# Performance work log

Measured on AMD Instinct MI355X. Metric: run time of the kernel, lower is better.

## Reference

```python
import jax, jax.numpy as jnp
import numpy as np

B, T, E, H = 16, 1024, 1024, 16
DH = E // H  # 64, divisible by 4
THETA = 10000.0


def setup_inputs() -> dict:
    key = jax.random.key(0)
    ks = jax.random.split(key, 10)
    inp = {
        "hidden_states": jax.random.normal(ks[0], (B, T, E), dtype=jnp.float32),
        "rope_pos": jax.random.randint(ks[1], (B, T, 2), 0, 32, dtype=jnp.int32),
    }
    s = 0.02
    inp["Wq"] = jax.random.normal(ks[2], (E, E), dtype=jnp.float32) * s
    inp["bq"] = jnp.zeros((E,), dtype=jnp.float32)
    inp["Wk"] = jax.random.normal(ks[3], (E, E), dtype=jnp.float32) * s
    inp["bk"] = jnp.zeros((E,), dtype=jnp.float32)
    inp["Wv"] = jax.random.normal(ks[4], (E, E), dtype=jnp.float32) * s
    inp["bv"] = jnp.zeros((E,), dtype=jnp.float32)
    inp["Wo"] = jax.random.normal(ks[5], (E, E), dtype=jnp.float32) * s
    inp["bo"] = jnp.zeros((E,), dtype=jnp.float32)
    return inp


def _rotate_half(x):
    # interleaved pairs: (x0,x1,x2,x3,...) -> (-x1,x0,-x3,x2,...)
    x_even = x[..., ::2]
    x_odd = x[..., 1::2]
    return jnp.stack((-x_odd, x_even), axis=-1).reshape(x.shape)


def _apply_rope_2d(q, k, rope_pos, theta):
    Dh = q.shape[-1]
    half, quarter = Dh // 2, Dh // 4
    dtype = q.dtype
    idx = jnp.arange(quarter, dtype=dtype)
    inv = (theta ** (-2.0 * idx / quarter)).astype(dtype)  # [quarter]
    pos_h = rope_pos[..., 0].astype(dtype)[..., None]  # [B,T,1]
    pos_w = rope_pos[..., 1].astype(dtype)[..., None]
    ang_h = pos_h * inv  # [B,T,quarter]
    ang_w = pos_w * inv
    ri = lambda a: jnp.repeat(a, 2, axis=-1)[:, None]  # -> [B,1,T,half]
    cos_h, sin_h = ri(jnp.cos(ang_h)), ri(jnp.sin(ang_h))
    cos_w, sin_w = ri(jnp.cos(ang_w)), ri(jnp.sin(ang_w))
    q_h, q_w = q[..., :half], q[..., half:]
    k_h, k_w = k[..., :half], k[..., half:]
    q_h = q_h * cos_h + _rotate_half(q_h) * sin_h
    k_h = k_h * cos_h + _rotate_half(k_h) * sin_h
    q_w = q_w * cos_w + _rotate_half(q_w) * sin_w
    k_w = k_w * cos_w + _rotate_half(k_w) * sin_w
    return jnp.concatenate([q_h, q_w], axis=-1), jnp.concatenate([k_h, k_w], axis=-1)


def reference(hidden_states, rope_pos, Wq, bq, Wk, bk, Wv, bv, Wo, bo):
    b, t, e = hidden_states.shape
    scale = DH ** -0.5
    # torch nn.Linear: y = x @ W.T + b, W is [out, in]
    proj = lambda x, W, bias: jnp.einsum('bte,oe->bto', x, W) + bias
    q = proj(hidden_states, Wq, bq).reshape(b, t, H, DH).transpose(0, 2, 1, 3)
    k = proj(hidden_states, Wk, bk).reshape(b, t, H, DH).transpose(0, 2, 1, 3)
    v = proj(hidden_states, Wv, bv).reshape(b, t, H, DH).transpose(0, 2, 1, 3)
    q, k = _apply_rope_2d(q, k, rope_pos, THETA)
    # eager attention: scores in input dtype, softmax in float32
    scores = jnp.einsum('bhqd,bhkd->bhqk', q, k) * scale
    w = jax.nn.softmax(scores.astype(jnp.float32), axis=-1).astype(q.dtype)
    out = jnp.einsum('bhqk,bhkd->bhqd', w, v)
    out = out.transpose(0, 2, 1, 3).reshape(b, t, e)
    return jnp.einsum('bte,oe->bto', out, Wo) + bo
```

## Files before the change

### kernel.cpp

```cpp
#include <hip/hip_runtime.h>
#include <hip/hip_bf16.h>

#define B_  16
#define T_  1024
#define E_  1024
#define H_  16
#define DH_ 64

typedef short s16x8 __attribute__((ext_vector_type(8)));
typedef float f32x4 __attribute__((ext_vector_type(4)));
typedef unsigned short u16x4 __attribute__((ext_vector_type(4)));

__device__ __forceinline__ void async_cp16(const void* g, void* l) {
  __builtin_amdgcn_global_load_lds(
      (__attribute__((address_space(1))) unsigned int*)(g),
      (__attribute__((address_space(3))) unsigned int*)(l), 16, 0, 0);
}

__device__ __forceinline__ s16x8 frag8(const void* p) { return *(const s16x8*)p; }

__device__ __forceinline__ float fexp2(float x) {
#if __has_builtin(__builtin_amdgcn_exp2f)
  return __builtin_amdgcn_exp2f(x);
#else
  return exp2f(x);
#endif
}

__device__ __forceinline__ unsigned short f2bu(float x) {
  __hip_bfloat16 h = __float2bfloat16(x);
  return *reinterpret_cast<unsigned short*>(&h);
}

__global__ __launch_bounds__(256) void cast_all(const float* __restrict__ X,
                                                const float* __restrict__ Wq,
                                                const float* __restrict__ Wk,
                                                const float* __restrict__ Wv,
                                                const float* __restrict__ Wo,
                                                __hip_bfloat16* __restrict__ Xb,
                                                __hip_bfloat16* __restrict__ Wqkvb,
                                                __hip_bfloat16* __restrict__ Wob) {
  const int bid = blockIdx.x;
  const float* src;
  __hip_bfloat16* dst;
  int i;
  if (bid < 16384) {
    src = X; dst = Xb;
    i = ((bid & 7) * 2048 + (bid >> 3)) * 256 + threadIdx.x;
  } else {
    const int wb = bid - 16384;
    const int w = wb >> 10;
    src = (w == 0) ? Wq : (w == 1) ? Wk : (w == 2) ? Wv : Wo;
    dst = (w == 3) ? Wob : Wqkvb + (size_t)w * 1048576;
    i = (wb & 1023) * 256 + threadIdx.x;
  }
  float4 v = ((const float4*)src)[i];
  u16x4 pk = {f2bu(v.x), f2bu(v.y), f2bu(v.z), f2bu(v.w)};
  *(u16x4*)(dst + (size_t)i * 4) = pk;
}

#define G8_ISSUE(SRC_, LOFF_, H_, D_, KT_)                                      \
  {                                                                             \
    _Pragma("unroll") for (int u_ = 0; u_ < 2; ++u_) {                          \
      const int ch_ = u_ * 8 + wave;                                            \
      async_cp16(SRC_ + (size_t)((H_)*128 + ch_ * 8) * 2048 + (KT_)*128,        \
                 smem + (D_)*65536 + (LOFF_) + (H_)*16384 + ch_ * 1024);        \
    }                                                                           \
  }

#define G8_READ_A(D_, S_)                                                       \
  {                                                                             \
    _Pragma("unroll") for (int i_ = 0; i_ < 4; ++i_) {                          \
      const char* rp_ = smem + (D_)*65536 + wrow * 16384 +                      \
                        ((S_)*64 + i_ * 16 + col) * 128;                        \
      af[i_][0] = frag8(rp_ + sw0);                                             \
      af[i_][1] = frag8(rp_ + sw1);                                             \
    }                                                                           \
  }

#define G8_READ_B(D_, T8_, BF_)                                                 \
  {                                                                             \
    _Pragma("unroll") for (int j_ = 0; j_ < 2; ++j_) {                          \
      const char* rp_ = smem + (D_)*65536 + 32768 + (wcol >> 1) * 16384 +       \
                        ((wcol & 1) * 64 + (T8_)*32 + j_ * 16 + col) * 128;     \
      BF_[j_][0] = frag8(rp_ + sw0);                                            \
      BF_[j_][1] = frag8(rp_ + sw1);                                            \
    }                                                                           \
  }

#define G8_MFMA(S_, T8_, BF_)                                                   \
  {                                                                             \
    __builtin_amdgcn_s_setprio(1);                                              \
    _Pragma("unroll") for (int i_ = 0; i_ < 4; ++i_)                            \
      _Pragma("unroll") for (int j_ = 0; j_ < 2; ++j_) {                        \
        acc[(S_)*4 + i_][(T8_)*2 + j_] = __builtin_amdgcn_mfma_f32_16x16x32_bf16( \
            af[i_][0], BF_[j_][0], acc[(S_)*4 + i_][(T8_)*2 + j_], 0, 0, 0);    \
        acc[(S_)*4 + i_][(T8_)*2 + j_] = __builtin_amdgcn_mfma_f32_16x16x32_bf16( \
            af[i_][1], BF_[j_][1], acc[(S_)*4 + i_][(T8_)*2 + j_], 0, 0, 0);    \
      }                                                                         \
    __builtin_amdgcn_s_setprio(0);                                              \
  }

#define G8_KTILE(D_, GA_, GB_, KTA_, KTB_, VM_)                                 \
  G8_READ_A(D_, 0)                                                              \
  G8_READ_B(D_, 0, bf0)                                                         \
  if (GA_) G8_ISSUE(Asrc, 0, 0, (D_) ^ 1, KTA_)                                 \
  __builtin_amdgcn_s_barrier();                                                 \
  G8_MFMA(0, 0, bf0)                                                            \
  __builtin_amdgcn_s_barrier();                                                 \
  G8_READ_B(D_, 1, bf1)                                                         \
  if (GA_) G8_ISSUE(Asrc, 0, 1, (D_) ^ 1, KTA_)                                 \
  __builtin_amdgcn_s_barrier();                                                 \
  G8_MFMA(0, 1, bf1)                                                            \
  __builtin_amdgcn_s_barrier();                                                 \
  G8_READ_A(D_, 1)                                                              \
  if (GB_) G8_ISSUE(Bsrc, 32768, 0, (D_), KTB_)                                 \
  __builtin_amdgcn_s_barrier();                                                 \
  G8_MFMA(1, 1, bf1)                                                            \
  __builtin_amdgcn_s_barrier();                                                 \
  if (GB_) G8_ISSUE(Bsrc, 32768, 1, (D_), KTB_)                                 \
  __builtin_amdgcn_s_barrier();                                                 \
  G8_MFMA(1, 0, bf0)                                                            \
  if (VM_) { asm volatile("s_waitcnt vmcnt(4)" ::: "memory"); }                 \
  else     { asm volatile("s_waitcnt vmcnt(0)" ::: "memory"); }                 \
  __builtin_amdgcn_s_barrier();

#define G8_CORE(APTR_, BPTR_)                                                   \
  __shared__ __align__(16) char smem[131072];                                   \
  const int tid = threadIdx.x;                                                  \
  const int lane = tid & 63, wave = tid >> 6;                                   \
  const int col = lane & 15, quad = lane >> 4;                                  \
  const int wrow = wave >> 2, wcol = wave & 3;                                  \
  const int r8 = lane >> 3;                                                     \
  const int gsw = (lane & 7) ^ r8;                                              \
  const int sw0 = (quad ^ (col & 7)) * 16;                                      \
  const int sw1 = ((quad + 4) ^ (col & 7)) * 16;                                \
  const char* Asrc = (const char*)(APTR_) + (size_t)(bm + r8) * 2048 + gsw * 16;\
  const char* Bsrc = (const char*)(BPTR_) + (size_t)(bn + r8) * 2048 + gsw * 16;\
  const f32x4 fzero = {0.f, 0.f, 0.f, 0.f};                                     \
  f32x4 acc[8][4];                                                              \
  _Pragma("unroll") for (int i_ = 0; i_ < 8; i_++)                              \
    _Pragma("unroll") for (int j_ = 0; j_ < 4; j_++) acc[i_][j_] = fzero;       \
  s16x8 af[4][2], bf0[2][2], bf1[2][2];                                         \
  G8_ISSUE(Bsrc, 32768, 0, 0, 0)                                                \
  G8_ISSUE(Bsrc, 32768, 1, 0, 0)                                                \
  G8_ISSUE(Asrc, 0, 0, 0, 0)                                                    \
  G8_ISSUE(Asrc, 0, 1, 0, 0)                                                    \
  G8_ISSUE(Bsrc, 32768, 0, 1, 1)                                                \
  G8_ISSUE(Bsrc, 32768, 1, 1, 1)                                                \
  asm volatile("s_waitcnt vmcnt(4)" ::: "memory");                              \
  __builtin_amdgcn_s_barrier();                                                 \
  _Pragma("clang loop unroll(disable)") for (int it = 0; it < 8; ++it) {        \
    const bool g7 = (it < 7);                                                   \
    G8_KTILE(0, true, g7, 2 * it + 1, 2 * it + 2, g7)                           \
    G8_KTILE(1, g7, g7, 2 * it + 2, 2 * it + 3, g7)                             \
  }

__global__ __launch_bounds__(512, 2) void gemm_qkv(const __hip_bfloat16* __restrict__ A,
                                                   const __hip_bfloat16* __restrict__ Wqkv,
                                                   const float* __restrict__ bq,
                                                   const float* __restrict__ bk,
                                                   const float* __restrict__ bv,
                                                   const int* __restrict__ pos,
                                                   __hip_bfloat16* __restrict__ Qb,
                                                   __hip_bfloat16* __restrict__ Kb,
                                                   __hip_bfloat16* __restrict__ Vt) {
  const int xcd = blockIdx.x & 7, s = blockIdx.x >> 3;
  const int bm = (xcd * 8 + (s & 7)) << 8;
  const int bn = (s >> 3) << 8;
  G8_CORE(A, Wqkv)

  const int seg = bn >> 10;
  const float* bp = (seg == 0) ? bq : (seg == 1) ? bk : bv;
  const int nbase = (bn & 1023) + wcol * 64;
  float bcol[4];
#pragma unroll
  for (int j = 0; j < 4; j++) bcol[j] = bp[nbase + j * 16 + col];
  if (seg < 2) {
    __syncthreads();
    float2* tab = (float2*)smem;
    {
      const int p_ = tid >> 4, f_ = tid & 15;
      const float inv = __expf((float)f_ * -1.1512925464970229f);
      float s_, c_;
      __sincosf((float)p_ * inv, &s_, &c_);
      tab[tid] = make_float2(c_, s_);
    }
    __syncthreads();
    const float SCL = (seg == 0) ? 0.18033688011112043f : 1.0f;
    __hip_bfloat16* P = (seg == 0) ? Qb : Kb;
    const int codd = col & 1;
#pragma unroll
    for (int mi = 0; mi < 8; mi++) {
      const int gr0 = bm + wrow * 128 + mi * 16 + quad * 4;
#pragma unroll
      for (int r = 0; r < 4; r++) {
        const int grow = gr0 + r;
        const int2 pp = *(const int2*)&pos[grow * 2];
        const int iph = pp.x, ipw = pp.y;
#pragma unroll
        for (int ni = 0; ni < 4; ni++) {
          const int f = ((ni & 1) << 3) + (col >> 1);
          const int p_ = (ni >= 2) ? ipw : iph;
          const float2 cs = tab[p_ * 16 + f];
          const float v = acc[mi][ni][r] + bcol[ni];
          const float vp = __shfl_xor(v, 1, 64);
          const float rot = codd ? (v * cs.x + vp * cs.y) : (v * cs.x - vp * cs.y);
          P[(size_t)grow * 1024 + nbase + ni * 16 + col] = __float2bfloat16(rot * SCL);
        }
      }
    }
  } else {
#pragma unroll
    for (int mi = 0; mi < 8; mi++) {
      const int gr0 = bm + wrow * 128 + mi * 16 + quad * 4;
      const int bb = gr0 >> 10, tt = gr0 & 1023;
#pragma unroll
      for (int ni = 0; ni < 4; ni++) {
        const int nc = nbase + ni * 16 + col;
        const int hh = nc >> 6, dd = nc & 63;
        u16x4 pk = {f2bu(acc[mi][ni][0] + bcol[ni]), f2bu(acc[mi][ni][1] + bcol[ni]),
                    f2bu(acc[mi][ni][2] + bcol[ni]), f2bu(acc[mi][ni][3] + bcol[ni])};
        *(u16x4*)(Vt + (((size_t)bb * H_ + hh) * DH_ + dd) * T_ + tt) = pk;
      }
    }
  }
}

__global__ __launch_bounds__(512, 2) void gemm_out(const __hip_bfloat16* __restrict__ A,
                                                   const __hip_bfloat16* __restrict__ Bw,
                                                   const float* __restrict__ bias,
                                                   float* __restrict__ Cout) {
  const int xcd = blockIdx.x & 7, s = blockIdx.x >> 3;
  const int bm = (xcd * 8 + (s & 7)) << 8;
  const int bn = (s >> 3) << 8;
  G8_CORE(A, Bw)

  const int nbase = bn + wcol * 64;
  float bcol[4];
#pragma unroll
  for (int j = 0; j < 4; j++) bcol[j] = bias[nbase + j * 16 + col];
#pragma unroll
  for (int mi = 0; mi < 8; mi++) {
    const int gr0 = bm + wrow * 128 + mi * 16 + quad * 4;
#pragma unroll
    for (int ni = 0; ni < 4; ni++) {
      const int gcol = nbase + ni * 16 + col;
#pragma unroll
      for (int r = 0; r < 4; r++)
        Cout[(size_t)(gr0 + r) * 1024 + gcol] = acc[mi][ni][r] + bcol[ni];
    }
  }
}

__global__ __launch_bounds__(256, 3) void attn_flash(const __hip_bfloat16* __restrict__ Q,
                                                     const __hip_bfloat16* __restrict__ Kt,
                                                     const __hip_bfloat16* __restrict__ Vt,
                                                     __hip_bfloat16* __restrict__ Oa) {
  __shared__ __align__(16) char QP[128 * 128];
  __shared__ __align__(16) char KV[2][2][8192];

  const int bid = blockIdx.x;
  const int xcd = bid & 7, slot = bid >> 3;
  const int bh = xcd * 32 + (slot >> 3);
  const int qt = slot & 7;
  const int b = bh >> 4, h = bh & 15;
  const int tid = threadIdx.x;
  const int lane = tid & 63, wave = tid >> 6;
  const int col = lane & 15, quad = lane >> 4;
  const int r8 = lane >> 3;
  const int gsw = ((lane & 7) ^ r8) * 16;
  const int sw0 = (quad ^ (col & 7)) * 16;
  const int sw1 = ((quad + 4) ^ (col & 7)) * 16;

  const size_t qrow0 = (size_t)b * T_ + qt * 128;

  const char* Kbase = (const char*)(Kt + (size_t)b * T_ * E_ + h * DH_);
  const char* Vbase = (const char*)(Vt + ((size_t)b * H_ + h) * DH_ * (size_t)T_);
#define STAGE_KV(KB_, D_)                                                          \
  {                                                                                \
    _Pragma("unroll") for (int u_ = 0; u_ < 2; ++u_) {                             \
      const int ch_ = u_ * 4 + wave;                                               \
      async_cp16(Kbase + (size_t)((KB_) + ch_ * 8 + r8) * 2048 + gsw,              \
                 &KV[D_][0][ch_ * 1024]);                                          \
      async_cp16(Vbase + (size_t)(ch_ * 8 + r8) * 2048 + (KB_)*2 + gsw,            \
                 &KV[D_][1][ch_ * 1024]);                                          \
    }                                                                              \
  }

  STAGE_KV(0, 0)
#pragma unroll
  for (int cc = 0; cc < 4; ++cc) {
    int c = tid + cc * 256;
    int r = c >> 3, k8 = c & 7;
    const float4* src = (const float4*)((const char*)(Q + (qrow0 + r) * E_ + h * DH_)) + k8;
    *(float4*)(QP + r * 128 + ((k8 ^ (r & 7)) << 4)) = *src;
  }
  __syncthreads();

  s16x8 qf[2][2];
#pragma unroll
  for (int g = 0; g < 2; g++) {
    const char* qp = QP + (g * 64 + wave * 16 + col) * 128;
    qf[g][0] = frag8(qp + sw0);
    qf[g][1] = frag8(qp + sw1);
  }
  __syncthreads();

  const f32x4 fzero = {0.f, 0.f, 0.f, 0.f};
  f32x4 o[2][4];
  float lr[2] = {0.f, 0.f};
#pragma unroll
  for (int g = 0; g < 2; g++)
#pragma unroll
    for (int j = 0; j < 4; j++) o[g][j] = fzero;
  char* Pw = QP + wave * 32 * 128;

  for (int kt2 = 0; kt2 < 16; ++kt2) {
    const int d = kt2 & 1;
    if (kt2 < 15) STAGE_KV((kt2 + 1) * 64, d ^ 1)
    s16x8 kf[4][2];
#pragma unroll
    for (int ktile = 0; ktile < 4; ktile++) {
      const char* kp = &KV[d][0][(ktile * 16 + col) * 128];
      kf[ktile][0] = frag8(kp + sw0);
      kf[ktile][1] = frag8(kp + sw1);
    }
    __builtin_amdgcn_s_setprio(1);
#pragma unroll
    for (int g = 0; g < 2; g++) {
#pragma unroll
      for (int ktile = 0; ktile < 4; ktile++) {
        f32x4 dacc = fzero;
        dacc = __builtin_amdgcn_mfma_f32_16x16x32_bf16(kf[ktile][0], qf[g][0], dacc, 0, 0, 0);
        dacc = __builtin_amdgcn_mfma_f32_16x16x32_bf16(kf[ktile][1], qf[g][1], dacc, 0, 0, 0);
        float p0 = fexp2(dacc[0]), p1 = fexp2(dacc[1]), p2 = fexp2(dacc[2]), p3 = fexp2(dacc[3]);
        lr[g] += (p0 + p1) + (p2 + p3);
        u16x4 pk = {f2bu(p0), f2bu(p1), f2bu(p2), f2bu(p3)};
        *(u16x4*)(Pw + (g * 16 + col) * 128 +
                  (((ktile * 2 + (quad >> 1)) ^ (col & 7)) << 4) + ((quad & 1) << 3)) = pk;
      }
    }
    __builtin_amdgcn_s_setprio(0);
    s16x8 vf[4][2];
#pragma unroll
    for (int jm = 0; jm < 4; jm++) {
      const char* vp = &KV[d][1][(jm * 16 + col) * 128];
      vf[jm][0] = frag8(vp + sw0);
      vf[jm][1] = frag8(vp + sw1);
    }
    __builtin_amdgcn_s_setprio(1);
#pragma unroll
    for (int g = 0; g < 2; g++) {
      const char* pp = Pw + (g * 16 + col) * 128;
      s16x8 pf0 = frag8(pp + sw0);
      s16x8 pf1 = frag8(pp + sw1);
#pragma unroll
      for (int jm = 0; jm < 4; jm++) {
        o[g][jm] = __builtin_amdgcn_mfma_f32_16x16x32_bf16(vf[jm][0], pf0, o[g][jm], 0, 0, 0);
        o[g][jm] = __builtin_amdgcn_mfma_f32_16x16x32_bf16(vf[jm][1], pf1, o[g][jm], 0, 0, 0);
      }
    }
    __builtin_amdgcn_s_setprio(0);
    __syncthreads();
  }
#undef STAGE_KV
#pragma unroll
  for (int g = 0; g < 2; g++) {
    lr[g] += __shfl_xor(lr[g], 16, 64);
    lr[g] += __shfl_xor(lr[g], 32, 64);
  }
#pragma unroll
  for (int g = 0; g < 2; g++) {
    float invl = 1.f / lr[g];
    size_t grow = qrow0 + g * 64 + wave * 16 + col;
    char* obase = (char*)(Oa + grow * E_ + h * DH_);
#pragma unroll
    for (int jm = 0; jm < 4; jm++) {
      u16x4 pk = {f2bu(o[g][jm][0] * invl), f2bu(o[g][jm][1] * invl),
                  f2bu(o[g][jm][2] * invl), f2bu(o[g][jm][3] * invl)};
      *(u16x4*)(obase + jm * 32 + quad * 8) = pk;
    }
  }
}

extern "C" void kernel_launch(void* const* d_in, const int* in_sizes, int n_in,
                              void* d_out, int out_size, void* d_ws, size_t ws_size,
                              hipStream_t stream) {
  const float* X   = (const float*)d_in[0];
  const int*   pos = (const int*)d_in[1];
  const float* Wq  = (const float*)d_in[2];
  const float* bq  = (const float*)d_in[3];
  const float* Wk  = (const float*)d_in[4];
  const float* bk  = (const float*)d_in[5];
  const float* Wv  = (const float*)d_in[6];
  const float* bv  = (const float*)d_in[7];
  const float* Wo  = (const float*)d_in[8];
  const float* bo  = (const float*)d_in[9];
  float* out = (float*)d_out;

  char* ws = (char*)d_ws;
  const size_t MB = 1024 * 1024;
  __hip_bfloat16* Xb    = (__hip_bfloat16*)(ws + 0 * MB);
  __hip_bfloat16* Qb    = (__hip_bfloat16*)(ws + 32 * MB);
  __hip_bfloat16* Kb    = (__hip_bfloat16*)(ws + 64 * MB);
  __hip_bfloat16* Vtb   = (__hip_bfloat16*)(ws + 96 * MB);
  __hip_bfloat16* Wqkvb = (__hip_bfloat16*)(ws + 128 * MB);
  __hip_bfloat16* Wob   = (__hip_bfloat16*)(ws + 136 * MB);
  __hip_bfloat16* Ab    = Xb;

  cast_all<<<20480, 256, 0, stream>>>(X, Wq, Wk, Wv, Wo, Xb, Wqkvb, Wob);

  gemm_qkv<<<768, 512, 0, stream>>>(Xb, Wqkvb, bq, bk, bv, pos, Qb, Kb, Vtb);

  attn_flash<<<2048, 256, 0, stream>>>(Qb, Kb, Vtb, Ab);

  gemm_out<<<256, 512, 0, stream>>>(Ab, Wob, bo, out);
}
```

Baseline: 366.4 us.

## Replace 256x256 GEMM tiles with 256x128 tiles and triple-buffered K=32 pipeline

Both projection GEMMs switch from 256x256 output tiles with 128-wide K stages and double buffering to 256x128 tiles with 32-wide K stages in a three-buffer async-copy ring. Shared memory drops from 128KB to 72KB and accumulators halve, raising launch bounds to 4 blocks per CU and doubling grid sizes for better occupancy and load balance. The trade-off is lower per-block data reuse and more barriers per unit of K work.

Result: no change. 367.4 us (+0.3%).

```diff
diff --git a/kernel.cpp b/kernel.cpp
--- a/kernel.cpp
+++ b/kernel.cpp
@@ -59,104 +59,74 @@
   *(u16x4*)(dst + (size_t)i * 4) = pk;
 }
 
-#define G8_ISSUE(SRC_, LOFF_, H_, D_, KT_)                                      \
+#define T3_ISSUE(SRC_, LOFF_, D_, KT2_, NCH_)                                   \
   {                                                                             \
-    _Pragma("unroll") for (int u_ = 0; u_ < 2; ++u_) {                          \
+    _Pragma("unroll") for (int u_ = 0; u_ < (NCH_); ++u_) {                     \
       const int ch_ = u_ * 8 + wave;                                            \
-      async_cp16(SRC_ + (size_t)((H_)*128 + ch_ * 8) * 2048 + (KT_)*128,        \
-                 smem + (D_)*65536 + (LOFF_) + (H_)*16384 + ch_ * 1024);        \
+      async_cp16(SRC_ + (size_t)(ch_ * 16) * 2048 + (KT2_)*64,                  \
+                 smem + (D_)*24576 + (LOFF_) + ch_ * 1024);                     \
     }                                                                           \
   }
 
-#define G8_READ_A(D_, S_)                                                       \
+#define T3_READ(D_)                                                             \
   {                                                                             \
-    _Pragma("unroll") for (int i_ = 0; i_ < 4; ++i_) {                          \
-      const char* rp_ = smem + (D_)*65536 + wrow * 16384 +                      \
-                        ((S_)*64 + i_ * 16 + col) * 128;                        \
-      af[i_][0] = frag8(rp_ + sw0);                                             \
-      af[i_][1] = frag8(rp_ + sw1);                                             \
-    }                                                                           \
-  }
-
-#define G8_READ_B(D_, T8_, BF_)                                                 \
-  {                                                                             \
-    _Pragma("unroll") for (int j_ = 0; j_ < 2; ++j_) {                          \
-      const char* rp_ = smem + (D_)*65536 + 32768 + (wcol >> 1) * 16384 +       \
-                        ((wcol & 1) * 64 + (T8_)*32 + j_ * 16 + col) * 128;     \
-      BF_[j_][0] = frag8(rp_ + sw0);                                            \
-      BF_[j_][1] = frag8(rp_ + sw1);                                            \
-    }                                                                           \
-  }
-
-#define G8_MFMA(S_, T8_, BF_)                                                   \
+    _Pragma("unroll") for (int i_ = 0; i_ < 4; ++i_)                            \
+      af[i_] = frag8(smem + (D_)*24576 + (wrow * 64 + i_ * 16 + col) * 64 + swk); \
+    _Pragma("unroll") for (int j_ = 0; j_ < 4; ++j_)                            \
+      bf[j_] = frag8(smem + (D_)*24576 + 16384 + (wcol * 64 + j_ * 16 + col) * 64 + swk); \
+  }
+
+#define T3_MFMA()                                                               \
   {                                                                             \
     __builtin_amdgcn_s_setprio(1);                                              \
     _Pragma("unroll") for (int i_ = 0; i_ < 4; ++i_)                            \
-      _Pragma("unroll") for (int j_ = 0; j_ < 2; ++j_) {                        \
-        acc[(S_)*4 + i_][(T8_)*2 + j_] = __builtin_amdgcn_mfma_f32_16x16x32_bf16( \
-            af[i_][0], BF_[j_][0], acc[(S_)*4 + i_][(T8_)*2 + j_], 0, 0, 0);    \
-        acc[(S_)*4 + i_][(T8_)*2 + j_] = __builtin_amdgcn_mfma_f32_16x16x32_bf16( \
-            af[i_][1], BF_[j_][1], acc[(S_)*4 + i_][(T8_)*2 + j_], 0, 0, 0);    \
-      }                                                                         \
+      _Pragma("unroll") for (int j_ = 0; j_ < 4; ++j_)                          \
+        acc[i_][j_] = __builtin_amdgcn_mfma_f32_16x16x32_bf16(af[i_], bf[j_], acc[i_][j_], 0, 0, 0); \
     __builtin_amdgcn_s_setprio(0);                                              \
   }
 
-#define G8_KTILE(D_, GA_, GB_, KTA_, KTB_, VM_)                                 \
-  G8_READ_A(D_, 0)                                                              \
-  G8_READ_B(D_, 0, bf0)                                                         \
-  if (GA_) G8_ISSUE(Asrc, 0, 0, (D_) ^ 1, KTA_)                                 \
+#define T3_KTILE(BUF_, GI_, IBUF_, KT2_, W_)                                    \
+  if (GI_) {                                                                    \
+    T3_ISSUE(Asrc, 0, IBUF_, KT2_, 2)                                           \
+    T3_ISSUE(Bsrc, 16384, IBUF_, KT2_, 1)                                       \
+  }                                                                             \
+  T3_READ(BUF_)                                                                 \
   __builtin_amdgcn_s_barrier();                                                 \
-  G8_MFMA(0, 0, bf0)                                                            \
-  __builtin_amdgcn_s_barrier();                                                 \
-  G8_READ_B(D_, 1, bf1)                                                         \
-  if (GA_) G8_ISSUE(Asrc, 0, 1, (D_) ^ 1, KTA_)                                 \
-  __builtin_amdgcn_s_barrier();                                                 \
-  G8_MFMA(0, 1, bf1)                                                            \
-  __builtin_amdgcn_s_barrier();                                                 \
-  G8_READ_A(D_, 1)                                                              \
-  if (GB_) G8_ISSUE(Bsrc, 32768, 0, (D_), KTB_)                                 \
-  __builtin_amdgcn_s_barrier();                                                 \
-  G8_MFMA(1, 1, bf1)                                                            \
-  __builtin_amdgcn_s_barrier();                                                 \
-  if (GB_) G8_ISSUE(Bsrc, 32768, 1, (D_), KTB_)                                 \
-  __builtin_amdgcn_s_barrier();                                                 \
-  G8_MFMA(1, 0, bf0)                                                            \
-  if (VM_) { asm volatile("s_waitcnt vmcnt(4)" ::: "memory"); }                 \
-  else     { asm volatile("s_waitcnt vmcnt(0)" ::: "memory"); }                 \
+  T3_MFMA()                                                                     \
+  asm volatile("s_waitcnt vmcnt(" #W_ ")" ::: "memory");                        \
   __builtin_amdgcn_s_barrier();
 
-#define G8_CORE(APTR_, BPTR_)                                                   \
-  __shared__ __align__(16) char smem[131072];                                   \
+#define T3_CORE(APTR_, BPTR_)                                                   \
+  __shared__ __align__(16) char smem[73728];                                    \
   const int tid = threadIdx.x;                                                  \
   const int lane = tid & 63, wave = tid >> 6;                                   \
   const int col = lane & 15, quad = lane >> 4;                                  \
-  const int wrow = wave >> 2, wcol = wave & 3;                                  \
-  const int r8 = lane >> 3;                                                     \
-  const int gsw = (lane & 7) ^ r8;                                              \
-  const int sw0 = (quad ^ (col & 7)) * 16;                                      \
-  const int sw1 = ((quad + 4) ^ (col & 7)) * 16;                                \
-  const char* Asrc = (const char*)(APTR_) + (size_t)(bm + r8) * 2048 + gsw * 16;\
-  const char* Bsrc = (const char*)(BPTR_) + (size_t)(bn + r8) * 2048 + gsw * 16;\
+  const int wrow = wave >> 1, wcol = wave & 1;                                  \
+  const int r4 = lane >> 2;                                                     \
+  const int gsw = (lane & 3) ^ ((lane >> 3) & 3);                               \
+  const int swk = (quad ^ ((col >> 1) & 3)) * 16;                               \
+  const char* Asrc = (const char*)(APTR_) + (size_t)(bm + r4) * 2048 + gsw * 16;\
+  const char* Bsrc = (const char*)(BPTR_) + (size_t)(bn + r4) * 2048 + gsw * 16;\
   const f32x4 fzero = {0.f, 0.f, 0.f, 0.f};                                     \
-  f32x4 acc[8][4];                                                              \
-  _Pragma("unroll") for (int i_ = 0; i_ < 8; i_++)                              \
+  f32x4 acc[4][4];                                                              \
+  _Pragma("unroll") for (int i_ = 0; i_ < 4; i_++)                              \
     _Pragma("unroll") for (int j_ = 0; j_ < 4; j_++) acc[i_][j_] = fzero;       \
-  s16x8 af[4][2], bf0[2][2], bf1[2][2];                                         \
-  G8_ISSUE(Bsrc, 32768, 0, 0, 0)                                                \
-  G8_ISSUE(Bsrc, 32768, 1, 0, 0)                                                \
-  G8_ISSUE(Asrc, 0, 0, 0, 0)                                                    \
-  G8_ISSUE(Asrc, 0, 1, 0, 0)                                                    \
-  G8_ISSUE(Bsrc, 32768, 0, 1, 1)                                                \
-  G8_ISSUE(Bsrc, 32768, 1, 1, 1)                                                \
-  asm volatile("s_waitcnt vmcnt(4)" ::: "memory");                              \
+  s16x8 af[4], bf[4];                                                           \
+  T3_ISSUE(Asrc, 0, 0, 0, 2)                                                    \
+  T3_ISSUE(Bsrc, 16384, 0, 0, 1)                                                \
+  T3_ISSUE(Asrc, 0, 1, 1, 2)                                                    \
+  T3_ISSUE(Bsrc, 16384, 1, 1, 1)                                                \
+  asm volatile("s_waitcnt vmcnt(3)" ::: "memory");                              \
   __builtin_amdgcn_s_barrier();                                                 \
-  _Pragma("clang loop unroll(disable)") for (int it = 0; it < 8; ++it) {        \
-    const bool g7 = (it < 7);                                                   \
-    G8_KTILE(0, true, g7, 2 * it + 1, 2 * it + 2, g7)                           \
-    G8_KTILE(1, g7, g7, 2 * it + 2, 2 * it + 3, g7)                             \
-  }
-
-__global__ __launch_bounds__(512, 2) void gemm_qkv(const __hip_bfloat16* __restrict__ A,
+  _Pragma("clang loop unroll(disable)") for (int it = 0; it < 10; ++it) {       \
+    T3_KTILE(0, true, 2, 3 * it + 2, 3)                                         \
+    T3_KTILE(1, true, 0, 3 * it + 3, 3)                                         \
+    T3_KTILE(2, true, 1, 3 * it + 4, 3)                                         \
+  }                                                                             \
+  T3_KTILE(0, false, 0, 0, 0)                                                   \
+  T3_KTILE(1, false, 0, 0, 0)
+
+__global__ __launch_bounds__(512, 4) void gemm_qkv(const __hip_bfloat16* __restrict__ A,
                                                    const __hip_bfloat16* __restrict__ Wqkv,
                                                    const float* __restrict__ bq,
                                                    const float* __restrict__ bk,
@@ -167,8 +137,8 @@
                                                    __hip_bfloat16* __restrict__ Vt) {
   const int xcd = blockIdx.x & 7, s = blockIdx.x >> 3;
   const int bm = (xcd * 8 + (s & 7)) << 8;
-  const int bn = (s >> 3) << 8;
-  G8_CORE(A, Wqkv)
+  const int bn = (s >> 3) << 7;
+  T3_CORE(A, Wqkv)
 
   const int seg = bn >> 10;
   const float* bp = (seg == 0) ? bq : (seg == 1) ? bk : bv;
@@ -191,8 +161,8 @@
     __hip_bfloat16* P = (seg == 0) ? Qb : Kb;
     const int codd = col & 1;
 #pragma unroll
-    for (int mi = 0; mi < 8; mi++) {
-      const int gr0 = bm + wrow * 128 + mi * 16 + quad * 4;
+    for (int mi = 0; mi < 4; mi++) {
+      const int gr0 = bm + wrow * 64 + mi * 16 + quad * 4;
 #pragma unroll
       for (int r = 0; r < 4; r++) {
         const int grow = gr0 + r;
@@ -212,8 +182,8 @@
     }
   } else {
 #pragma unroll
-    for (int mi = 0; mi < 8; mi++) {
-      const int gr0 = bm + wrow * 128 + mi * 16 + quad * 4;
+    for (int mi = 0; mi < 4; mi++) {
+      const int gr0 = bm + wrow * 64 + mi * 16 + quad * 4;
       const int bb = gr0 >> 10, tt = gr0 & 1023;
 #pragma unroll
       for (int ni = 0; ni < 4; ni++) {
@@ -227,22 +197,22 @@
   }
 }
 
-__global__ __launch_bounds__(512, 2) void gemm_out(const __hip_bfloat16* __restrict__ A,
+__global__ __launch_bounds__(512, 4) void gemm_out(const __hip_bfloat16* __restrict__ A,
                                                    const __hip_bfloat16* __restrict__ Bw,
                                                    const float* __restrict__ bias,
                                                    float* __restrict__ Cout) {
   const int xcd = blockIdx.x & 7, s = blockIdx.x >> 3;
   const int bm = (xcd * 8 + (s & 7)) << 8;
-  const int bn = (s >> 3) << 8;
-  G8_CORE(A, Bw)
+  const int bn = (s >> 3) << 7;
+  T3_CORE(A, Bw)
 
   const int nbase = bn + wcol * 64;
   float bcol[4];
 #pragma unroll
   for (int j = 0; j < 4; j++) bcol[j] = bias[nbase + j * 16 + col];
 #pragma unroll
-  for (int mi = 0; mi < 8; mi++) {
-    const int gr0 = bm + wrow * 128 + mi * 16 + quad * 4;
+  for (int mi = 0; mi < 4; mi++) {
+    const int gr0 = bm + wrow * 64 + mi * 16 + quad * 4;
 #pragma unroll
     for (int ni = 0; ni < 4; ni++) {
       const int gcol = nbase + ni * 16 + col;
@@ -411,9 +381,9 @@
 
   cast_all<<<20480, 256, 0, stream>>>(X, Wq, Wk, Wv, Wo, Xb, Wqkvb, Wob);
 
-  gemm_qkv<<<768, 512, 0, stream>>>(Xb, Wqkvb, bq, bk, bv, pos, Qb, Kb, Vtb);
+  gemm_qkv<<<1536, 512, 0, stream>>>(Xb, Wqkvb, bq, bk, bv, pos, Qb, Kb, Vtb);
 
   attn_flash<<<2048, 256, 0, stream>>>(Qb, Kb, Vtb, Ab);
 
-  gemm_out<<<256, 512, 0, stream>>>(Ab, Wob, bo, out);
-}
+  gemm_out<<<512, 512, 0, stream>>>(Ab, Wob, bo, out);
+}
```
